# Kernel tuning notes

Measured on AMD Instinct MI355X. Metric: run time of the kernel, lower is better.

The kernel has to match this reference:

```python
import jax, jax.numpy as jnp
import numpy as np

# Model dims (match init_kwargs)
E = 512        # embed_dim
H = 8          # n_heads
L = 6          # n_layers
DFF = 2048     # PyTorch TransformerEncoderLayer default dim_feedforward
K = 1024       # codebook_size
V = 32         # num_joints
NQ = 1         # n_q
T = 64         # frames
B = 2
MAX_T = 512    # time_pos table size
LN_EPS = 1e-5


def make_block_causal_mask(t, v):
    """True=keep. Causal across frames, full attention within a frame."""
    s = t * v
    i = np.arange(s)
    tril = i[:, None] >= i[None, :]
    same_frame = (i[:, None] // v) == (i[None, :] // v)
    return jnp.asarray(tril | same_frame)


def setup_inputs() -> dict:
    key = jax.random.key(0)
    ks = jax.random.split(key, 20)
    sc = 0.02
    inp = {
        "indices": jax.random.randint(ks[0], (B, T, V, NQ), 0, K, dtype=jnp.int64 if jax.config.jax_enable_x64 else jnp.int32),
        "attention_mask": make_block_causal_mask(T, V),
        # embedding tables
        "code_emb": jax.random.normal(ks[1], (K, E), jnp.float32) * sc,
        "stage_emb": jax.random.normal(ks[2], (NQ, E), jnp.float32) * sc,
        "time_pos": jax.random.normal(ks[3], (MAX_T, E), jnp.float32) * sc,
        "joint_pos": jax.random.normal(ks[4], (V, E), jnp.float32) * sc,
        # per-layer stacked transformer params
        "in_proj_w": jax.random.normal(ks[5], (L, 3 * E, E), jnp.float32) * sc,
        "in_proj_b": jnp.zeros((L, 3 * E), jnp.float32),
        "out_w": jax.random.normal(ks[6], (L, E, E), jnp.float32) * sc,
        "out_b": jnp.zeros((L, E), jnp.float32),
        "ln1_g": jnp.ones((L, E), jnp.float32),
        "ln1_b": jnp.zeros((L, E), jnp.float32),
        "lin1_w": jax.random.normal(ks[7], (L, DFF, E), jnp.float32) * sc,
        "lin1_b": jnp.zeros((L, DFF), jnp.float32),
        "lin2_w": jax.random.normal(ks[8], (L, E, DFF), jnp.float32) * sc,
        "lin2_b": jnp.zeros((L, E), jnp.float32),
        "ln2_g": jnp.ones((L, E), jnp.float32),
        "ln2_b": jnp.zeros((L, E), jnp.float32),
    }
    return inp


def _ln(x, g, b):
    mu = jnp.mean(x, axis=-1, keepdims=True)
    var = jnp.mean(jnp.square(x - mu), axis=-1, keepdims=True)
    return (x - mu) * jax.lax.rsqrt(var + LN_EPS) * g + b


def _mha(x, keep, wi, bi, wo, bo):
    Bq, S, _ = x.shape
    dh = E // H
    qkv = x @ wi.T + bi                       # [B,S,3E]
    q, k, v = jnp.split(qkv, 3, axis=-1)
    q = q.reshape(Bq, S, H, dh)
    k = k.reshape(Bq, S, H, dh)
    v = v.reshape(Bq, S, H, dh)
    scores = jnp.einsum('bqhd,bkhd->bhqk', q, k) / jnp.sqrt(jnp.float32(dh))
    scores = jnp.where(keep[None, None], scores, jnp.float32(-1e30))
    attn = jax.nn.softmax(scores, axis=-1)
    o = jnp.einsum('bhqk,bkhd->bqhd', attn, v).reshape(Bq, S, E)
    return o @ wo.T + bo


def _transformer(indices, keep, code_emb, stage_emb, time_pos, joint_pos,
                 in_proj_w, in_proj_b, out_w, out_b, ln1_g, ln1_b,
                 lin1_w, lin1_b, lin2_w, lin2_b, ln2_g, ln2_b):
    Bq, Tq, Vq, nq = indices.shape
    emb = code_emb[indices] + stage_emb[None, None, None]       # [B,T,V,nq,E]
    emb = emb.reshape(Bq, Tq, Vq * nq, E)
    v_ids = jnp.repeat(jnp.arange(Vq), nq)
    emb = emb + time_pos[:Tq][None, :, None, :] + joint_pos[v_ids][None, None, :, :]
    x = emb.reshape(Bq, Tq * Vq * nq, E)
    for l in range(L):
        y = _ln(x, ln1_g[l], ln1_b[l])
        x = x + _mha(y, keep, in_proj_w[l], in_proj_b[l], out_w[l], out_b[l])
        y = _ln(x, ln2_g[l], ln2_b[l])
        h = jax.nn.gelu(y @ lin1_w[l].T + lin1_b[l], approximate=False)
        x = x + h @ lin2_w[l].T + lin2_b[l]
    return x.reshape(Bq, Tq, Vq * nq, E)


def reference(indices, attention_mask, code_emb, stage_emb, time_pos, joint_pos,
              in_proj_w, in_proj_b, out_w, out_b, ln1_g, ln1_b,
              lin1_w, lin1_b, lin2_w, lin2_b, ln2_g, ln2_b):
    # attention_mask is [T*V, T*V] with n_q=1, so no repeat_interleave needed.
    keep = attention_mask
    if NQ > 1 and attention_mask.shape[0] == T * V:
        keep = jnp.repeat(jnp.repeat(attention_mask, NQ, 0), NQ, 1)
    return _transformer(indices, keep, code_emb, stage_emb, time_pos, joint_pos,
                        in_proj_w, in_proj_b, out_w, out_b, ln1_g, ln1_b,
                        lin1_w, lin1_b, lin2_w, lin2_b, ln2_g, ln2_b)
```

## Files before the change

### kernel.cpp

```cpp
#include <hip/hip_runtime.h>
#include <hip/hip_bf16.h>
#include <math.h>

#define E 512
#define H_HEADS 8
#define DH 64
#define NLAYER 6
#define DFF 2048
#define SEQ 2048
#define NB 2
#define M_TOK (NB*SEQ)

typedef float f32x4_t __attribute__((ext_vector_type(4)));
typedef __bf16 bf16x8_t __attribute__((ext_vector_type(8)));
typedef short s16x8_t __attribute__((ext_vector_type(8)));

__device__ __forceinline__ short f2bf(float f) {
    union { float f; unsigned u; } v; v.f = f;
    unsigned r = v.u + 0x7FFFu + ((v.u >> 16) & 1u);
    return (short)(r >> 16);
}
__device__ __forceinline__ float bf2f(short s) {
    union { unsigned u; float f; } v; v.u = ((unsigned)(unsigned short)s) << 16;
    return v.f;
}

__device__ __forceinline__ bf16x8_t mk_frag(short4 lo, short4 hi) {
    s16x8_t t;
    t[0] = lo.x; t[1] = lo.y; t[2] = lo.z; t[3] = lo.w;
    t[4] = hi.x; t[5] = hi.y; t[6] = hi.z; t[7] = hi.w;
    return __builtin_bit_cast(bf16x8_t, t);
}

__device__ __forceinline__ void gload16(const void* g, void* l) {
    __builtin_amdgcn_global_load_lds(
        (const __attribute__((address_space(1))) void*)g,
        (__attribute__((address_space(3))) void*)l, 16, 0, 0);
}

__global__ __launch_bounds__(256) void embed_kernel(
    const int* __restrict__ idx, const float* __restrict__ ce,
    const float* __restrict__ se, const float* __restrict__ tp,
    const float* __restrict__ jp, float* __restrict__ x)
{
    int i = blockIdx.x * 256 + threadIdx.x;
    int e4 = i & 127;
    int row = i >> 7;
    int v = row & 31;
    int t = (row >> 5) & 63;
    int code = idx[row];
    const float4* ce4 = (const float4*)ce;
    const float4* se4 = (const float4*)se;
    const float4* tp4 = (const float4*)tp;
    const float4* jp4 = (const float4*)jp;
    float4 a = ce4[code * 128 + e4];
    float4 b = se4[e4];
    float4 c = tp4[t * 128 + e4];
    float4 d = jp4[v * 128 + e4];
    float4 o;
    o.x = a.x + b.x + c.x + d.x;
    o.y = a.y + b.y + c.y + d.y;
    o.z = a.z + b.z + c.z + d.z;
    o.w = a.w + b.w + c.w + d.w;
    ((float4*)x)[i] = o;
}

__global__ __launch_bounds__(256) void cast4_kernel(
    const float* __restrict__ w0, const float* __restrict__ w1,
    const float* __restrict__ w2, const float* __restrict__ w3,
    short* __restrict__ o)
{
    int i = blockIdx.x * 256 + threadIdx.x;
    const float* src; int off;
    if (i < 98304)       { src = w0; off = i; }
    else if (i < 131072) { src = w1; off = i - 98304; }
    else if (i < 262144) { src = w2; off = i - 131072; }
    else                 { src = w3; off = i - 262144; }
    float4 a = ((const float4*)src)[off * 2];
    float4 b = ((const float4*)src)[off * 2 + 1];
    s16x8_t s;
    s[0] = f2bf(a.x); s[1] = f2bf(a.y); s[2] = f2bf(a.z); s[3] = f2bf(a.w);
    s[4] = f2bf(b.x); s[5] = f2bf(b.y); s[6] = f2bf(b.z); s[7] = f2bf(b.w);
    *(s16x8_t*)&o[(size_t)i * 8] = s;
}

__global__ __launch_bounds__(256) void ln_kernel(
    const float* __restrict__ x, short* __restrict__ y,
    const float* __restrict__ g, const float* __restrict__ b)
{
    int wave = threadIdx.x >> 6;
    int lane = threadIdx.x & 63;
    int row = blockIdx.x * 4 + wave;
    const float4* xr = (const float4*)(x + (size_t)row * E);
    float4 v0 = xr[lane];
    float4 v1 = xr[lane + 64];
    float s  = v0.x + v0.y + v0.z + v0.w + v1.x + v1.y + v1.z + v1.w;
    float ss = v0.x*v0.x + v0.y*v0.y + v0.z*v0.z + v0.w*v0.w
             + v1.x*v1.x + v1.y*v1.y + v1.z*v1.z + v1.w*v1.w;
    #pragma unroll
    for (int off = 32; off; off >>= 1) {
        s  += __shfl_xor(s, off, 64);
        ss += __shfl_xor(ss, off, 64);
    }
    float mu = s * (1.f / E);
    float var = ss * (1.f / E) - mu * mu;
    float rs = rsqrtf(var + 1e-5f);
    const float4* g4 = (const float4*)g;
    const float4* b4 = (const float4*)b;
    float4 gg = g4[lane], bb = b4[lane];
    short4 o;
    o.x = f2bf((v0.x - mu) * rs * gg.x + bb.x);
    o.y = f2bf((v0.y - mu) * rs * gg.y + bb.y);
    o.z = f2bf((v0.z - mu) * rs * gg.z + bb.z);
    o.w = f2bf((v0.w - mu) * rs * gg.w + bb.w);
    *(short4*)&y[(size_t)row * E + lane * 4] = o;
    gg = g4[lane + 64]; bb = b4[lane + 64];
    o.x = f2bf((v1.x - mu) * rs * gg.x + bb.x);
    o.y = f2bf((v1.y - mu) * rs * gg.y + bb.y);
    o.z = f2bf((v1.z - mu) * rs * gg.z + bb.z);
    o.w = f2bf((v1.w - mu) * rs * gg.w + bb.w);
    *(short4*)&y[(size_t)row * E + 256 + lane * 4] = o;
}

template<int MODE>
__global__ __launch_bounds__(256) void gemm_mfma_kernel(
    const short* __restrict__ A, const short* __restrict__ W,
    const float* __restrict__ bias, const float* __restrict__ res,
    void* __restrict__ out, int N, int K)
{
    __shared__ short As[128 * 64];
    __shared__ short Bs[128 * 64];
    int nb = N >> 7;
    int bx = blockIdx.x % nb;
    int by = blockIdx.x / nb;
    int tid = threadIdx.x;
    int lane = tid & 63, g = lane >> 4, l16 = lane & 15;
    int w = tid >> 6, wm = w >> 1, wn = w & 1;
    int wbase = tid & 192;

    f32x4_t acc[4][4] = {};
    const short* Ab = A + (size_t)(by * 128) * K;
    const short* Wb = W + (size_t)(bx * 128) * K;

    for (int k0 = 0; k0 < K; k0 += 64) {
        __syncthreads();
        #pragma unroll
        for (int u = 0; u < 4; ++u) {
            int c = u * 256 + tid;
            int row = c >> 3, c8 = c & 7;
            gload16(Ab + (size_t)row * K + k0 + c8 * 8, As + (u * 256 + wbase) * 8);
            gload16(Wb + (size_t)row * K + k0 + c8 * 8, Bs + (u * 256 + wbase) * 8);
        }
        __syncthreads();
        #pragma unroll
        for (int ks = 0; ks < 2; ++ks) {
            bf16x8_t af[4], bf[4];
            #pragma unroll
            for (int i = 0; i < 4; ++i) {
                af[i] = *(const bf16x8_t*)&As[(wm * 64 + i * 16 + l16) * 64 + ks * 32 + g * 8];
                bf[i] = *(const bf16x8_t*)&Bs[(wn * 64 + i * 16 + l16) * 64 + ks * 32 + g * 8];
            }
            #pragma unroll
            for (int mi = 0; mi < 4; ++mi)
                #pragma unroll
                for (int ni = 0; ni < 4; ++ni)
                    acc[mi][ni] = __builtin_amdgcn_mfma_f32_16x16x32_bf16(
                        af[mi], bf[ni], acc[mi][ni], 0, 0, 0);
        }
    }

    int gm0 = by * 128 + wm * 64;
    int gn0 = bx * 128 + wn * 64;
    #pragma unroll
    for (int ni = 0; ni < 4; ++ni) {
        int gn = gn0 + ni * 16 + l16;
        float bv = bias[gn];
        #pragma unroll
        for (int mi = 0; mi < 4; ++mi) {
            #pragma unroll
            for (int r = 0; r < 4; ++r) {
                int gm = gm0 + mi * 16 + g * 4 + r;
                float v = acc[mi][ni][r] + bv;
                if (MODE == 2) v = 0.5f * v * (1.f + erff(v * 0.70710678118f));
                if (MODE == 1) {
                    v += res[(size_t)gm * N + gn];
                    ((float*)out)[(size_t)gm * N + gn] = v;
                } else {
                    ((short*)out)[(size_t)gm * N + gn] = f2bf(v);
                }
            }
        }
    }
}

__global__ __launch_bounds__(128) void attn_mfma_kernel(
    const short* __restrict__ qkv, short* __restrict__ opart,
    float* __restrict__ mlbuf)
{
    __shared__ __align__(16) char smem[13312];
    short* Qs = (short*)smem;
    short* Ks = (short*)(smem + 4352);
    short* Vt = (short*)(smem + 8704);
    float* Ol = (float*)smem;

    int bid = blockIdx.x;
    int c   = bid & 3;
    int qb  = 63 - ((bid >> 2) & 63);
    int bh  = bid >> 8;
    if (c * 16 > qb) return;
    int h = bh & 7, b = bh >> 3;
    int a_ = qb >> 4, r_ = qb & 15;
    int cidx = bh * 160 + (a_ + 1) * (8 * a_ + r_) + c;

    int tid  = threadIdx.x;
    int w    = tid >> 6;
    int lane = tid & 63;
    int g    = lane >> 4;
    int l16  = lane & 15;

    const short* base = qkv + (size_t)(b * SEQ) * 1536;

    #pragma unroll
    for (int u = 0; u < 4; ++u) {
        int f = tid + 128 * u;
        int qr = f >> 4, c4 = f & 15;
        short4 v = *(const short4*)(base + (size_t)(qb * 32 + qr) * 1536 + h * 64 + c4 * 4);
        *(short4*)&Qs[qr * 68 + c4 * 4] = v;
    }

    int kstart = c * 512;
    int kcend  = min((qb + 1) * 32, kstart + 512);

    short4 kreg[4], vreg[4];
    #pragma unroll
    for (int u = 0; u < 4; ++u) {
        int f = tid + 128 * u;
        int key = f >> 4, c4 = f & 15;
        const short* row = base + (size_t)(kstart + key) * 1536 + h * 64;
        kreg[u] = *(const short4*)(row + 512 + c4 * 4);
        vreg[u] = *(const short4*)(row + 1024 + c4 * 4);
    }
    __syncthreads();

    bf16x8_t qf[2];
    #pragma unroll
    for (int ks = 0; ks < 2; ++ks) {
        const short* qrow = &Qs[(w * 16 + l16) * 68];
        short4 lo = *(const short4*)&qrow[4 * g + 32 * ks];
        short4 hi = *(const short4*)&qrow[4 * g + 16 + 32 * ks];
        qf[ks] = mk_frag(lo, hi);
    }

    f32x4_t oa[4] = {};
    float mrun = -1e30f, lrun = 0.f;

    for (int kt = kstart; kt < kcend; kt += 32) {
        __syncthreads();
        #pragma unroll
        for (int u = 0; u < 4; ++u) {
            int f = tid + 128 * u;
            int key = f >> 4, c4 = f & 15;
            *(short4*)&Ks[key * 68 + c4 * 4] = kreg[u];
            Vt[(c4 * 4 + 0) * 36 + key] = vreg[u].x;
            Vt[(c4 * 4 + 1) * 36 + key] = vreg[u].y;
            Vt[(c4 * 4 + 2) * 36 + key] = vreg[u].z;
            Vt[(c4 * 4 + 3) * 36 + key] = vreg[u].w;
        }
        if (kt + 32 < kcend) {
            #pragma unroll
            for (int u = 0; u < 4; ++u) {
                int f = tid + 128 * u;
                int key = f >> 4, c4 = f & 15;
                const short* row = base + (size_t)(kt + 32 + key) * 1536 + h * 64;
                kreg[u] = *(const short4*)(row + 512 + c4 * 4);
                vreg[u] = *(const short4*)(row + 1024 + c4 * 4);
            }
        }
        __syncthreads();

        f32x4_t st[2];
        __builtin_amdgcn_s_setprio(1);
        #pragma unroll
        for (int mt = 0; mt < 2; ++mt) {
            f32x4_t acc = {0.f, 0.f, 0.f, 0.f};
            #pragma unroll
            for (int ks = 0; ks < 2; ++ks) {
                const short* krow = &Ks[(mt * 16 + l16) * 68];
                short4 lo = *(const short4*)&krow[4 * g + 32 * ks];
                short4 hi = *(const short4*)&krow[4 * g + 16 + 32 * ks];
                acc = __builtin_amdgcn_mfma_f32_16x16x32_bf16(mk_frag(lo, hi), qf[ks], acc, 0, 0, 0);
            }
            st[mt] = acc;
        }
        __builtin_amdgcn_s_setprio(0);

        float s8[8];
        #pragma unroll
        for (int mt = 0; mt < 2; ++mt)
            #pragma unroll
            for (int r = 0; r < 4; ++r)
                s8[mt * 4 + r] = st[mt][r] * 0.125f;
        float tm = s8[0];
        #pragma unroll
        for (int j = 1; j < 8; ++j) tm = fmaxf(tm, s8[j]);
        tm = fmaxf(tm, __shfl_xor(tm, 16));
        tm = fmaxf(tm, __shfl_xor(tm, 32));
        float mnew = fmaxf(mrun, tm);
        float cf = __expf(mrun - mnew);
        mrun = mnew;
        float ps = 0.f;
        short pb[8];
        #pragma unroll
        for (int j = 0; j < 8; ++j) {
            float p = __expf(s8[j] - mrun);
            ps += p;
            pb[j] = f2bf(p);
        }
        ps += __shfl_xor(ps, 16);
        ps += __shfl_xor(ps, 32);
        lrun = lrun * cf + ps;
        #pragma unroll
        for (int dt = 0; dt < 4; ++dt)
            #pragma unroll
            for (int r = 0; r < 4; ++r)
                oa[dt][r] *= cf;
        s16x8_t pt;
        #pragma unroll
        for (int j = 0; j < 8; ++j) pt[j] = pb[j];
        bf16x8_t pf = __builtin_bit_cast(bf16x8_t, pt);

        __builtin_amdgcn_s_setprio(1);
        #pragma unroll
        for (int dt = 0; dt < 4; ++dt) {
            const short* vrow = &Vt[(dt * 16 + l16) * 36];
            short4 lo = *(const short4*)&vrow[4 * g];
            short4 hi = *(const short4*)&vrow[16 + 4 * g];
            oa[dt] = __builtin_amdgcn_mfma_f32_16x16x32_bf16(mk_frag(lo, hi), pf, oa[dt], 0, 0, 0);
        }
        __builtin_amdgcn_s_setprio(0);
    }

    __syncthreads();
    #pragma unroll
    for (int dt = 0; dt < 4; ++dt)
        #pragma unroll
        for (int r = 0; r < 4; ++r)
            Ol[(w * 16 + l16) * 68 + 16 * dt + 4 * g + r] = oa[dt][r];
    if (g == 0) {
        mlbuf[cidx * 64 + w * 16 + l16] = mrun;
        mlbuf[cidx * 64 + 32 + w * 16 + l16] = lrun;
    }
    int q = tid >> 2, d0 = (tid & 3) * 16;
    const float* orow = &Ol[q * 68 + d0];
    s16x8_t s0, s1;
    #pragma unroll
    for (int j = 0; j < 8; ++j) { s0[j] = f2bf(orow[j]); s1[j] = f2bf(orow[8 + j]); }
    size_t ob = (size_t)cidx * 2048 + q * 64 + d0;
    *(s16x8_t*)&opart[ob] = s0;
    *(s16x8_t*)&opart[ob + 8] = s1;
}

__global__ __launch_bounds__(128) void attn_combine_kernel(
    const short* __restrict__ opart, const float* __restrict__ mlbuf,
    short* __restrict__ y)
{
    int bid = blockIdx.x;
    int qb = bid & 63, bh = bid >> 6;
    int h = bh & 7, b = bh >> 3;
    int a_ = qb >> 4, r_ = qb & 15;
    int cbase = bh * 160 + (a_ + 1) * (8 * a_ + r_);
    int nc = a_ + 1;
    int t = threadIdx.x;
    int q = t >> 2, d0 = (t & 3) * 16;

    float M = -1e30f;
    #pragma unroll
    for (int cc = 0; cc < 4; ++cc)
        if (cc < nc) M = fmaxf(M, mlbuf[(cbase + cc) * 64 + q]);
    float L = 0.f;
    float acc[16] = {};
    #pragma unroll
    for (int cc = 0; cc < 4; ++cc) {
        if (cc < nc) {
            float mv = mlbuf[(cbase + cc) * 64 + q];
            float lv = mlbuf[(cbase + cc) * 64 + 32 + q];
            float wgt = __expf(mv - M);
            L += wgt * lv;
            const short* op = &opart[(size_t)(cbase + cc) * 2048 + q * 64 + d0];
            s16x8_t v0 = *(const s16x8_t*)op;
            s16x8_t v1 = *(const s16x8_t*)(op + 8);
            #pragma unroll
            for (int j = 0; j < 8; ++j) {
                acc[j]     += wgt * bf2f(v0[j]);
                acc[8 + j] += wgt * bf2f(v1[j]);
            }
        }
    }
    float inv = 1.f / L;
    s16x8_t o0, o1;
    #pragma unroll
    for (int j = 0; j < 8; ++j) { o0[j] = f2bf(acc[j] * inv); o1[j] = f2bf(acc[8 + j] * inv); }
    size_t gb = (size_t)(b * SEQ + qb * 32 + q) * E + h * 64 + d0;
    *(s16x8_t*)&y[gb] = o0;
    *(s16x8_t*)&y[gb + 8] = o1;
}

extern "C" void kernel_launch(void* const* d_in, const int* in_sizes, int n_in,
                              void* d_out, int out_size, void* d_ws, size_t ws_size,
                              hipStream_t stream) {
    const int*   idx = (const int*)d_in[0];
    const float* ce  = (const float*)d_in[2];
    const float* se  = (const float*)d_in[3];
    const float* tp  = (const float*)d_in[4];
    const float* jp  = (const float*)d_in[5];
    const float* ipw = (const float*)d_in[6];
    const float* ipb = (const float*)d_in[7];
    const float* ow  = (const float*)d_in[8];
    const float* ob  = (const float*)d_in[9];
    const float* l1g = (const float*)d_in[10];
    const float* l1b = (const float*)d_in[11];
    const float* w1  = (const float*)d_in[12];
    const float* b1  = (const float*)d_in[13];
    const float* w2  = (const float*)d_in[14];
    const float* b2  = (const float*)d_in[15];
    const float* l2g = (const float*)d_in[16];
    const float* l2b = (const float*)d_in[17];

    float* x = (float*)d_out;
    short* y_bf   = (short*)d_ws;
    short* qkv_bf = (short*)((char*)d_ws + (4u << 20));
    short* h_bf   = qkv_bf;
    short* wb     = (short*)((char*)d_ws + (20u << 20));
    short* wip = wb;
    short* wob = wb + 786432;
    short* w1b = wb + 1048576;
    short* w2b = wb + 2097152;
    short* opart = (short*)((char*)d_ws + (27u << 20));
    float* mlbuf = (float*)((char*)d_ws + (37u << 20));

    embed_kernel<<<2048, 256, 0, stream>>>(idx, ce, se, tp, jp, x);

    for (int l = 0; l < NLAYER; ++l) {
        cast4_kernel<<<1536, 256, 0, stream>>>(
            ipw + (size_t)l * 786432, ow + (size_t)l * 262144,
            w1 + (size_t)l * 1048576, w2 + (size_t)l * 1048576, wb);
        ln_kernel<<<1024, 256, 0, stream>>>(x, y_bf, l1g + l * E, l1b + l * E);
        gemm_mfma_kernel<0><<<32 * 12, 256, 0, stream>>>(
            y_bf, wip, ipb + (size_t)l * 1536, nullptr, qkv_bf, 1536, 512);
        attn_mfma_kernel<<<4096, 128, 0, stream>>>(qkv_bf, opart, mlbuf);
        attn_combine_kernel<<<1024, 128, 0, stream>>>(opart, mlbuf, y_bf);
        gemm_mfma_kernel<1><<<32 * 4, 256, 0, stream>>>(
            y_bf, wob, ob + (size_t)l * E, x, x, 512, 512);
        ln_kernel<<<1024, 256, 0, stream>>>(x, y_bf, l2g + l * E, l2b + l * E);
        gemm_mfma_kernel<2><<<32 * 16, 256, 0, stream>>>(
            y_bf, w1b, b1 + (size_t)l * DFF, nullptr, h_bf, 2048, 512);
        gemm_mfma_kernel<1><<<32 * 4, 256, 0, stream>>>(
            h_bf, w2b, b2 + (size_t)l * E, x, x, 512, 2048);
    }
}
```

Before: 1.225 ms.

## Write V transposed from QKV GEMM and load attention fragments directly from global

```diff
diff --git a/kernel.cpp b/kernel.cpp
--- a/kernel.cpp
+++ b/kernel.cpp
@@ -126,7 +126,7 @@
 __global__ __launch_bounds__(256) void gemm_mfma_kernel(
     const short* __restrict__ A, const short* __restrict__ W,
     const float* __restrict__ bias, const float* __restrict__ res,
-    void* __restrict__ out, int N, int K)
+    void* __restrict__ out, short* __restrict__ vt_out, int N, int K)
 {
     __shared__ short As[128 * 64];
     __shared__ short Bs[128 * 64];
@@ -177,31 +177,44 @@
         float bv = bias[gn];
         #pragma unroll
         for (int mi = 0; mi < 4; ++mi) {
+            float vals[4];
             #pragma unroll
             for (int r = 0; r < 4; ++r) {
-                int gm = gm0 + mi * 16 + g * 4 + r;
                 float v = acc[mi][ni][r] + bv;
                 if (MODE == 2) v = 0.5f * v * (1.f + erff(v * 0.70710678118f));
-                if (MODE == 1) {
-                    v += res[(size_t)gm * N + gn];
-                    ((float*)out)[(size_t)gm * N + gn] = v;
+                vals[r] = v;
+            }
+            int gmB = gm0 + mi * 16 + g * 4;
+            if (MODE == 3) {
+                if (gn < 1024) {
+                    #pragma unroll
+                    for (int r = 0; r < 4; ++r)
+                        ((short*)out)[(size_t)(gmB + r) * 1024 + gn] = f2bf(vals[r]);
                 } else {
-                    ((short*)out)[(size_t)gm * N + gn] = f2bf(v);
+                    short4 pk = { f2bf(vals[0]), f2bf(vals[1]), f2bf(vals[2]), f2bf(vals[3]) };
+                    int bb = gmB >> 11, ss = gmB & 2047;
+                    *(short4*)&vt_out[((size_t)(bb * 512 + (gn - 1024))) * 2048 + ss] = pk;
                 }
-            }
-        }
-    }
-}
-
-__global__ __launch_bounds__(128) void attn_mfma_kernel(
-    const short* __restrict__ qkv, short* __restrict__ opart,
-    float* __restrict__ mlbuf)
-{
-    __shared__ __align__(16) char smem[13312];
-    short* Qs = (short*)smem;
-    short* Ks = (short*)(smem + 4352);
-    short* Vt = (short*)(smem + 8704);
-    float* Ol = (float*)smem;
+            } else if (MODE == 1) {
+                #pragma unroll
+                for (int r = 0; r < 4; ++r) {
+                    float v = vals[r] + res[(size_t)(gmB + r) * N + gn];
+                    ((float*)out)[(size_t)(gmB + r) * N + gn] = v;
+                }
+            } else {
+                #pragma unroll
+                for (int r = 0; r < 4; ++r)
+                    ((short*)out)[(size_t)(gmB + r) * N + gn] = f2bf(vals[r]);
+            }
+        }
+    }
+}
+
+__global__ __launch_bounds__(64) void attn_mfma_kernel(
+    const short* __restrict__ qk, const short* __restrict__ vt,
+    short* __restrict__ opart, float* __restrict__ mlbuf)
+{
+    __shared__ __align__(16) float Ol[32 * 68];
 
     int bid = blockIdx.x;
     int c   = bid & 3;
@@ -212,152 +225,121 @@
     int a_ = qb >> 4, r_ = qb & 15;
     int cidx = bh * 160 + (a_ + 1) * (8 * a_ + r_) + c;
 
-    int tid  = threadIdx.x;
-    int w    = tid >> 6;
-    int lane = tid & 63;
-    int g    = lane >> 4;
-    int l16  = lane & 15;
-
-    const short* base = qkv + (size_t)(b * SEQ) * 1536;
-
-    #pragma unroll
-    for (int u = 0; u < 4; ++u) {
-        int f = tid + 128 * u;
-        int qr = f >> 4, c4 = f & 15;
-        short4 v = *(const short4*)(base + (size_t)(qb * 32 + qr) * 1536 + h * 64 + c4 * 4);
-        *(short4*)&Qs[qr * 68 + c4 * 4] = v;
-    }
+    int lane = threadIdx.x & 63;
+    int g = lane >> 4, l16 = lane & 15;
+
+    const short* qkb = qk + (size_t)(b * SEQ) * 1024;
+    const short* vb  = vt + (size_t)(bh * 64) * 2048;
+
+    bf16x8_t qf[2][2];
+    #pragma unroll
+    for (int qi = 0; qi < 2; ++qi)
+        #pragma unroll
+        for (int ks = 0; ks < 2; ++ks) {
+            const short* qrow = qkb + (size_t)(qb * 32 + qi * 16 + l16) * 1024 + h * 64;
+            short4 lo = *(const short4*)(qrow + 4 * g + 32 * ks);
+            short4 hi = *(const short4*)(qrow + 4 * g + 16 + 32 * ks);
+            qf[qi][ks] = mk_frag(lo, hi);
+        }
+
+    f32x4_t oa[2][4] = {};
+    float mrun[2] = {-1e30f, -1e30f}, lrun[2] = {0.f, 0.f};
 
     int kstart = c * 512;
     int kcend  = min((qb + 1) * 32, kstart + 512);
 
-    short4 kreg[4], vreg[4];
+    for (int kt = kstart; kt < kcend; kt += 32) {
+        bf16x8_t kf[2][2], vf[4];
+        #pragma unroll
+        for (int mt = 0; mt < 2; ++mt)
+            #pragma unroll
+            for (int ks = 0; ks < 2; ++ks) {
+                const short* krow = qkb + (size_t)(kt + mt * 16 + l16) * 1024 + 512 + h * 64;
+                short4 lo = *(const short4*)(krow + 4 * g + 32 * ks);
+                short4 hi = *(const short4*)(krow + 4 * g + 16 + 32 * ks);
+                kf[mt][ks] = mk_frag(lo, hi);
+            }
+        #pragma unroll
+        for (int dt = 0; dt < 4; ++dt) {
+            const short* vrow = vb + (size_t)(dt * 16 + l16) * 2048 + kt;
+            short4 lo = *(const short4*)(vrow + 4 * g);
+            short4 hi = *(const short4*)(vrow + 16 + 4 * g);
+            vf[dt] = mk_frag(lo, hi);
+        }
+
+        #pragma unroll
+        for (int qi = 0; qi < 2; ++qi) {
+            f32x4_t st[2];
+            #pragma unroll
+            for (int mt = 0; mt < 2; ++mt) {
+                f32x4_t acc = {0.f, 0.f, 0.f, 0.f};
+                #pragma unroll
+                for (int ks = 0; ks < 2; ++ks)
+                    acc = __builtin_amdgcn_mfma_f32_16x16x32_bf16(kf[mt][ks], qf[qi][ks], acc, 0, 0, 0);
+                st[mt] = acc;
+            }
+            float s8[8];
+            #pragma unroll
+            for (int mt = 0; mt < 2; ++mt)
+                #pragma unroll
+                for (int r = 0; r < 4; ++r)
+                    s8[mt * 4 + r] = st[mt][r] * 0.125f;
+            float tm = s8[0];
+            #pragma unroll
+            for (int j = 1; j < 8; ++j) tm = fmaxf(tm, s8[j]);
+            tm = fmaxf(tm, __shfl_xor(tm, 16));
+            tm = fmaxf(tm, __shfl_xor(tm, 32));
+            float mnew = fmaxf(mrun[qi], tm);
+            float cf = __expf(mrun[qi] - mnew);
+            mrun[qi] = mnew;
+            float ps = 0.f;
+            short pb[8];
+            #pragma unroll
+            for (int j = 0; j < 8; ++j) {
+                float p = __expf(s8[j] - mnew);
+                ps += p;
+                pb[j] = f2bf(p);
+            }
+            ps += __shfl_xor(ps, 16);
+            ps += __shfl_xor(ps, 32);
+            lrun[qi] = lrun[qi] * cf + ps;
+            #pragma unroll
+            for (int dt = 0; dt < 4; ++dt)
+                #pragma unroll
+                for (int r = 0; r < 4; ++r)
+                    oa[qi][dt][r] *= cf;
+            s16x8_t pt;
+            #pragma unroll
+            for (int j = 0; j < 8; ++j) pt[j] = pb[j];
+            bf16x8_t pf = __builtin_bit_cast(bf16x8_t, pt);
+            #pragma unroll
+            for (int dt = 0; dt < 4; ++dt)
+                oa[qi][dt] = __builtin_amdgcn_mfma_f32_16x16x32_bf16(vf[dt], pf, oa[qi][dt], 0, 0, 0);
+        }
+    }
+
+    #pragma unroll
+    for (int qi = 0; qi < 2; ++qi) {
+        #pragma unroll
+        for (int dt = 0; dt < 4; ++dt)
+            #pragma unroll
+            for (int r = 0; r < 4; ++r)
+                Ol[(qi * 16 + l16) * 68 + 16 * dt + 4 * g + r] = oa[qi][dt][r];
+        if (g == 0) {
+            mlbuf[cidx * 64 + qi * 16 + l16] = mrun[qi];
+            mlbuf[cidx * 64 + 32 + qi * 16 + l16] = lrun[qi];
+        }
+    }
+    int q = lane >> 1, d0 = (lane & 1) * 32;
+    const float* orow = &Ol[q * 68 + d0];
+    size_t ob = (size_t)cidx * 2048 + q * 64 + d0;
     #pragma unroll
     for (int u = 0; u < 4; ++u) {
-        int f = tid + 128 * u;
-        int key = f >> 4, c4 = f & 15;
-        const short* row = base + (size_t)(kstart + key) * 1536 + h * 64;
-        kreg[u] = *(const short4*)(row + 512 + c4 * 4);
-        vreg[u] = *(const short4*)(row + 1024 + c4 * 4);
-    }
-    __syncthreads();
-
-    bf16x8_t qf[2];
-    #pragma unroll
-    for (int ks = 0; ks < 2; ++ks) {
-        const short* qrow = &Qs[(w * 16 + l16) * 68];
-        short4 lo = *(const short4*)&qrow[4 * g + 32 * ks];
-        short4 hi = *(const short4*)&qrow[4 * g + 16 + 32 * ks];
-        qf[ks] = mk_frag(lo, hi);
-    }
-
-    f32x4_t oa[4] = {};
-    float mrun = -1e30f, lrun = 0.f;
-
-    for (int kt = kstart; kt < kcend; kt += 32) {
-        __syncthreads();
-        #pragma unroll
-        for (int u = 0; u < 4; ++u) {
-            int f = tid + 128 * u;
-            int key = f >> 4, c4 = f & 15;
-            *(short4*)&Ks[key * 68 + c4 * 4] = kreg[u];
-            Vt[(c4 * 4 + 0) * 36 + key] = vreg[u].x;
-            Vt[(c4 * 4 + 1) * 36 + key] = vreg[u].y;
-            Vt[(c4 * 4 + 2) * 36 + key] = vreg[u].z;
-            Vt[(c4 * 4 + 3) * 36 + key] = vreg[u].w;
-        }
-        if (kt + 32 < kcend) {
-            #pragma unroll
-            for (int u = 0; u < 4; ++u) {
-                int f = tid + 128 * u;
-                int key = f >> 4, c4 = f & 15;
-                const short* row = base + (size_t)(kt + 32 + key) * 1536 + h * 64;
-                kreg[u] = *(const short4*)(row + 512 + c4 * 4);
-                vreg[u] = *(const short4*)(row + 1024 + c4 * 4);
-            }
-        }
-        __syncthreads();
-
-        f32x4_t st[2];
-        __builtin_amdgcn_s_setprio(1);
-        #pragma unroll
-        for (int mt = 0; mt < 2; ++mt) {
-            f32x4_t acc = {0.f, 0.f, 0.f, 0.f};
-            #pragma unroll
-            for (int ks = 0; ks < 2; ++ks) {
-                const short* krow = &Ks[(mt * 16 + l16) * 68];
-                short4 lo = *(const short4*)&krow[4 * g + 32 * ks];
-                short4 hi = *(const short4*)&krow[4 * g + 16 + 32 * ks];
-                acc = __builtin_amdgcn_mfma_f32_16x16x32_bf16(mk_frag(lo, hi), qf[ks], acc, 0, 0, 0);
-            }
-            st[mt] = acc;
-        }
-        __builtin_amdgcn_s_setprio(0);
-
-        float s8[8];
-        #pragma unroll
-        for (int mt = 0; mt < 2; ++mt)
-            #pragma unroll
-            for (int r = 0; r < 4; ++r)
-                s8[mt * 4 + r] = st[mt][r] * 0.125f;
-        float tm = s8[0];
-        #pragma unroll
-        for (int j = 1; j < 8; ++j) tm = fmaxf(tm, s8[j]);
-        tm = fmaxf(tm, __shfl_xor(tm, 16));
-        tm = fmaxf(tm, __shfl_xor(tm, 32));
-        float mnew = fmaxf(mrun, tm);
-        float cf = __expf(mrun - mnew);
-        mrun = mnew;
-        float ps = 0.f;
-        short pb[8];
-        #pragma unroll
-        for (int j = 0; j < 8; ++j) {
-            float p = __expf(s8[j] - mrun);
-            ps += p;
-            pb[j] = f2bf(p);
-        }
-        ps += __shfl_xor(ps, 16);
-        ps += __shfl_xor(ps, 32);
-        lrun = lrun * cf + ps;
-        #pragma unroll
-        for (int dt = 0; dt < 4; ++dt)
-            #pragma unroll
-            for (int r = 0; r < 4; ++r)
-                oa[dt][r] *= cf;
-        s16x8_t pt;
-        #pragma unroll
-        for (int j = 0; j < 8; ++j) pt[j] = pb[j];
-        bf16x8_t pf = __builtin_bit_cast(bf16x8_t, pt);
-
-        __builtin_amdgcn_s_setprio(1);
-        #pragma unroll
-        for (int dt = 0; dt < 4; ++dt) {
-            const short* vrow = &Vt[(dt * 16 + l16) * 36];
-            short4 lo = *(const short4*)&vrow[4 * g];
-            short4 hi = *(const short4*)&vrow[16 + 4 * g];
-            oa[dt] = __builtin_amdgcn_mfma_f32_16x16x32_bf16(mk_frag(lo, hi), pf, oa[dt], 0, 0, 0);
-        }
-        __builtin_amdgcn_s_setprio(0);
-    }
-
-    __syncthreads();
-    #pragma unroll
-    for (int dt = 0; dt < 4; ++dt)
-        #pragma unroll
-        for (int r = 0; r < 4; ++r)
-            Ol[(w * 16 + l16) * 68 + 16 * dt + 4 * g + r] = oa[dt][r];
-    if (g == 0) {
-        mlbuf[cidx * 64 + w * 16 + l16] = mrun;
-        mlbuf[cidx * 64 + 32 + w * 16 + l16] = lrun;
-    }
-    int q = tid >> 2, d0 = (tid & 3) * 16;
-    const float* orow = &Ol[q * 68 + d0];
-    s16x8_t s0, s1;
-    #pragma unroll
-    for (int j = 0; j < 8; ++j) { s0[j] = f2bf(orow[j]); s1[j] = f2bf(orow[8 + j]); }
-    size_t ob = (size_t)cidx * 2048 + q * 64 + d0;
-    *(s16x8_t*)&opart[ob] = s0;
-    *(s16x8_t*)&opart[ob + 8] = s1;
+        s16x8_t sv;
+        #pragma unroll
+        for (int j = 0; j < 8; ++j) sv[j] = f2bf(orow[u * 8 + j]);
+        *(s16x8_t*)&opart[ob + u * 8] = sv;
+    }
 }
 
 __global__ __launch_bounds__(128) void attn_combine_kernel(
@@ -428,8 +410,9 @@
 
     float* x = (float*)d_out;
     short* y_bf   = (short*)d_ws;
-    short* qkv_bf = (short*)((char*)d_ws + (4u << 20));
-    short* h_bf   = qkv_bf;
+    short* qk_bf  = (short*)((char*)d_ws + (4u << 20));
+    short* vt_bf  = (short*)((char*)d_ws + (12u << 20));
+    short* h_bf   = qk_bf;
     short* wb     = (short*)((char*)d_ws + (20u << 20));
     short* wip = wb;
     short* wob = wb + 786432;
@@ -445,16 +428,16 @@
             ipw + (size_t)l * 786432, ow + (size_t)l * 262144,
             w1 + (size_t)l * 1048576, w2 + (size_t)l * 1048576, wb);
         ln_kernel<<<1024, 256, 0, stream>>>(x, y_bf, l1g + l * E, l1b + l * E);
-        gemm_mfma_kernel<0><<<32 * 12, 256, 0, stream>>>(
-            y_bf, wip, ipb + (size_t)l * 1536, nullptr, qkv_bf, 1536, 512);
-        attn_mfma_kernel<<<4096, 128, 0, stream>>>(qkv_bf, opart, mlbuf);
+        gemm_mfma_kernel<3><<<32 * 12, 256, 0, stream>>>(
+            y_bf, wip, ipb + (size_t)l * 1536, nullptr, qk_bf, vt_bf, 1536, 512);
+        attn_mfma_kernel<<<4096, 64, 0, stream>>>(qk_bf, vt_bf, opart, mlbuf);
         attn_combine_kernel<<<1024, 128, 0, stream>>>(opart, mlbuf, y_bf);
         gemm_mfma_kernel<1><<<32 * 4, 256, 0, stream>>>(
-            y_bf, wob, ob + (size_t)l * E, x, x, 512, 512);
+            y_bf, wob, ob + (size_t)l * E, x, x, nullptr, 512, 512);
         ln_kernel<<<1024, 256, 0, stream>>>(x, y_bf, l2g + l * E, l2b + l * E);
         gemm_mfma_kernel<2><<<32 * 16, 256, 0, stream>>>(
-            y_bf, w1b, b1 + (size_t)l * DFF, nullptr, h_bf, 2048, 512);
+            y_bf, w1b, b1 + (size_t)l * DFF, nullptr, h_bf, nullptr, 2048, 512);
         gemm_mfma_kernel<1><<<32 * 4, 256, 0, stream>>>(
-            h_bf, w2b, b2 + (size_t)l * E, x, x, 512, 2048);
-    }
-}
+            h_bf, w2b, b2 + (size_t)l * E, x, x, nullptr, 512, 2048);
+    }
+}
```

After: 1.574 ms. 1.28x slower.
